# Kernel tuning notes

Measured on AMD Instinct MI355X. Metric: run time of the kernel, lower is better.

The kernel has to match this reference:

```python
import jax, jax.numpy as jnp
import numpy as np

N = 50000      # nodes
E = 800000     # edges
D_IN = 128
D_OUT = 128
R = 8          # relation types
EPS = 1e-12    # F.normalize eps


def setup_inputs() -> dict:
    key = jax.random.key(0)
    ks = jax.random.split(key, 10)
    s_in = 1.0 / np.sqrt(D_IN)
    s_out = 1.0 / np.sqrt(D_OUT)
    return {
        "x": jax.random.normal(ks[0], (N, D_IN), jnp.float32),
        "W1": jax.random.normal(ks[1], (R, D_IN, D_OUT), jnp.float32) * s_in,
        "loopW1": jax.random.normal(ks[2], (D_IN, D_OUT), jnp.float32) * s_in,
        "b1": jax.random.normal(ks[3], (D_OUT,), jnp.float32) * 0.01,
        "W2": jax.random.normal(ks[4], (R, D_OUT, D_OUT), jnp.float32) * s_out,
        "loopW2": jax.random.normal(ks[5], (D_OUT, D_OUT), jnp.float32) * s_out,
        "b2": jax.random.normal(ks[6], (D_OUT,), jnp.float32) * 0.01,
        "src": jax.random.randint(ks[7], (E,), 0, N),
        "dst": jax.random.randint(ks[8], (E,), 0, N),
        "etypes": jax.random.randint(ks[9], (E,), 0, R),
    }


def rel_layer(x, src, dst, etypes, W, loopW, b):
    # transform every node by every relation: [R, N, D_out]
    xw = jnp.einsum('ni,rio->rno', x, W)
    # gather per-edge messages: [E, D_out]
    msg = xw[etypes, src]
    # scatter-add to destination nodes
    agg = jax.ops.segment_sum(msg, dst, num_segments=x.shape[0])
    # self-loop + bias (DGL RelGraphConv defaults)
    return agg + x @ loopW + b


def reference(x, W1, loopW1, b1, W2, loopW2, b2, src, dst, etypes):
    h = jax.nn.relu(rel_layer(x, src, dst, etypes, W1, loopW1, b1))
    h = rel_layer(h, src, dst, etypes, W2, loopW2, b2)
    # F.normalize: row-wise L2, eps=1e-12
    nrm = jnp.maximum(jnp.linalg.norm(h, axis=1, keepdims=True), EPS)
    return h / nrm
```

## Files before the change

### kernel.cpp

```cpp
#include <hip/hip_runtime.h>
#include <hip/hip_bf16.h>

#define D 128
#define CH 4096

typedef unsigned int u32;
typedef unsigned short u16;
typedef __attribute__((ext_vector_type(8))) short s16x8;
typedef __attribute__((ext_vector_type(4))) float f32x4;
typedef __attribute__((ext_vector_type(2))) float f32x2;

__device__ __forceinline__ float bf2f(u16 u) {
    union { u32 u; float f; } v; v.u = ((u32)u) << 16; return v.f;
}
__device__ __forceinline__ u16 f2bf(float f) {
    union { float f; u32 u; } v; v.f = f;
    return (u16)((v.u + 0x7fffu + ((v.u >> 16) & 1u)) >> 16);
}
__device__ __forceinline__ u32 pack_bf2(float a, float b) {
    __hip_bfloat162 t = __float22bfloat162_rn(make_float2(a, b));
    union { __hip_bfloat162 t; u32 u; } v; v.t = t; return v.u;
}
__device__ __forceinline__ void unpack2(u32 u, float& lo, float& hi) {
    union { u32 u; float f; } a, b;
    a.u = u << 16; b.u = u & 0xffff0000u;
    lo = a.f; hi = b.f;
}

__global__ void detect_dtype(const u16* __restrict__ x, int* __restrict__ flag) {
    __shared__ int cnt;
    if (threadIdx.x == 0) cnt = 0;
    __syncthreads();
    u16 u = x[2 * threadIdx.x];
    int e = (u >> 7) & 0xFF;
    if (e >= 96 && e <= 150) atomicAdd(&cnt, 1);
    __syncthreads();
    if (threadIdx.x == 0) *flag = (cnt >= 128) ? 0 : 1;
}

__global__ __launch_bounds__(256)
void to_bf16_all(const void* __restrict__ s0, const void* __restrict__ s1,
                 const void* __restrict__ s2, const void* __restrict__ s3,
                 const void* __restrict__ s4, const void* __restrict__ s5,
                 const void* __restrict__ s6,
                 u16* __restrict__ d0, u16* __restrict__ d1, u16* __restrict__ d2,
                 u16* __restrict__ d3, u16* __restrict__ d4, u16* __restrict__ d5,
                 u16* __restrict__ d6,
                 long long n0, long long n1, long long n2, long long n3,
                 long long n4, long long n5, long long n6,
                 const int* __restrict__ flag)
{
    if (*flag == 0) return;
    long long i = (long long)blockIdx.x * 256 + threadIdx.x;
    const void* s; u16* d; long long off;
    if      (i < n0)                   { s = s0; d = d0; off = i; }
    else if (i < n0+n1)                { s = s1; d = d1; off = i-n0; }
    else if (i < n0+n1+n2)             { s = s2; d = d2; off = i-n0-n1; }
    else if (i < n0+n1+n2+n3)          { s = s3; d = d3; off = i-n0-n1-n2; }
    else if (i < n0+n1+n2+n3+n4)       { s = s4; d = d4; off = i-n0-n1-n2-n3; }
    else if (i < n0+n1+n2+n3+n4+n5)    { s = s5; d = d5; off = i-n0-n1-n2-n3-n4; }
    else if (i < n0+n1+n2+n3+n4+n5+n6) { s = s6; d = d6; off = i-n0-n1-n2-n3-n4-n5; }
    else return;
    d[off] = f2bf(((const float*)s)[off]);
}

__global__ __launch_bounds__(256)
void zero_ints(int* __restrict__ a, int n) {
    int i = blockIdx.x * 256 + threadIdx.x;
    if (i < n) a[i] = 0;
}

__global__ __launch_bounds__(256)
void csr_count(const int* __restrict__ dst, int* __restrict__ gcnt, int E, int nbuck) {
    __shared__ int scnt[256];
    int tid = threadIdx.x;
    scnt[tid] = 0;
    __syncthreads();
    int base = blockIdx.x * CH;
#pragma unroll
    for (int it = 0; it < CH / 256; ++it) {
        int e = base + it * 256 + tid;
        if (e < E) atomicAdd(&scnt[dst[e] >> 8], 1);
    }
    __syncthreads();
    if (tid < nbuck && scnt[tid] > 0) atomicAdd(&gcnt[tid], scnt[tid]);
}

__global__ __launch_bounds__(256)
void csr_scan(const int* __restrict__ gcnt, int* __restrict__ bstart, int* __restrict__ bcur,
              int nbuck, int N_, int E_, int* __restrict__ offs) {
    __shared__ int wpart[4];
    int tid = threadIdx.x, lane = tid & 63, wid = tid >> 6;
    int v = (tid < nbuck) ? gcnt[tid] : 0;
    int s = v;
#pragma unroll
    for (int off = 1; off < 64; off <<= 1) {
        int t = __shfl_up(s, off, 64);
        if (lane >= off) s += t;
    }
    if (lane == 63) wpart[wid] = s;
    __syncthreads();
    int add = 0;
    for (int w = 0; w < wid; ++w) add += wpart[w];
    int excl = add + s - v;
    if (tid <= nbuck) bstart[tid] = excl;
    if (tid < nbuck)  bcur[tid]  = excl;
    if (tid == 0) offs[N_] = E_;
}

__global__ __launch_bounds__(256)
void csr_part(const int* __restrict__ src, const int* __restrict__ dst,
              const int* __restrict__ et, int* __restrict__ bcur,
              u32* __restrict__ ebuf, int E, int N, int nbuck) {
    __shared__ int scnt[256], sbase[256];
    int tid = threadIdx.x;
    scnt[tid] = 0;
    __syncthreads();
    int base = blockIdx.x * CH;
#pragma unroll
    for (int it = 0; it < CH / 256; ++it) {
        int e = base + it * 256 + tid;
        if (e < E) atomicAdd(&scnt[dst[e] >> 8], 1);
    }
    __syncthreads();
    if (tid < nbuck) {
        int c = scnt[tid];
        sbase[tid] = c ? atomicAdd(&bcur[tid], c) : 0;
    }
    __syncthreads();
    scnt[tid] = 0;
    __syncthreads();
#pragma unroll
    for (int it = 0; it < CH / 256; ++it) {
        int e = base + it * 256 + tid;
        if (e >= E) continue;
        int d = dst[e];
        int b = d >> 8;
        int p = sbase[b] + atomicAdd(&scnt[b], 1);
        ebuf[p] = ((u32)(d & 255) << 24) | (u32)(et[e] * N + src[e]);
    }
}

__global__ __launch_bounds__(256)
void csr_emit(const u32* __restrict__ ebuf, const int* __restrict__ bstart,
              int* __restrict__ offs, int* __restrict__ rowidx, int N) {
    __shared__ int hist[256], excl[256], cur[256];
    __shared__ int wpart[4];
    int b = blockIdx.x, tid = threadIdx.x;
    int lo = bstart[b], hi = bstart[b + 1];
    hist[tid] = 0; cur[tid] = 0;
    __syncthreads();
    for (int i = lo + tid; i < hi; i += 256) atomicAdd(&hist[ebuf[i] >> 24], 1);
    __syncthreads();
    int lane = tid & 63, wid = tid >> 6;
    int v = hist[tid], s = v;
#pragma unroll
    for (int off = 1; off < 64; off <<= 1) {
        int t = __shfl_up(s, off, 64);
        if (lane >= off) s += t;
    }
    if (lane == 63) wpart[wid] = s;
    __syncthreads();
    int add = 0;
    for (int w = 0; w < wid; ++w) add += wpart[w];
    int e_ = add + s - v;
    excl[tid] = e_;
    int node = (b << 8) + tid;
    if (node < N) offs[node] = lo + e_;
    __syncthreads();
    for (int i = lo + tid; i < hi; i += 256) {
        u32 rec = ebuf[i];
        int dl = rec >> 24;
        int p = lo + excl[dl] + atomicAdd(&cur[dl], 1);
        rowidx[p] = (int)(rec & 0xFFFFFFu);
    }
}

__global__ __launch_bounds__(256)
void gemm_k128(const u16* __restrict__ Ac, const u16* __restrict__ Ao,
               const u16* __restrict__ Wc, const u16* __restrict__ Wo,
               const u16* __restrict__ lWc, const u16* __restrict__ lWo,
               const u16* __restrict__ bc, const u16* __restrict__ bo,
               const int* __restrict__ flag,
               int M, int R_, u16* __restrict__ xw, u16* __restrict__ sl)
{
    __shared__ u16 As[128 * 128];
    const bool f = (*flag != 0);
    const u16* A     = f ? Ac  : Ao;
    const u16* Wall  = f ? Wc  : Wo;
    const u16* loopW = f ? lWc : lWo;
    const u16* bias  = f ? bc  : bo;

    const int y = blockIdx.y;
    const u16* B = (y < R_) ? (Wall + (long long)y * D * D) : loopW;
    const int row0 = blockIdx.x * 128;
    const int tid  = threadIdx.x;
    const int lane = tid & 63;
    const int wv   = tid >> 6;
    const int quad = lane >> 4;
    const int l16  = lane & 15;

    {
        int r_base = (wv << 2) + (lane >> 4);
        int c      = lane & 15;
        auto* lds0 = (__attribute__((address_space(3))) char*)As;
#pragma unroll
        for (int it = 0; it < 8; ++it) {
            int rl = it * 16 + r_base;
            int cg = c ^ (rl & 15);
            int rg = row0 + rl; if (rg >= M) rg = M - 1;
            const u16* gp = A + (long long)rg * D + cg * 8;
            __builtin_amdgcn_global_load_lds(
                (const __attribute__((address_space(1))) void*)gp,
                (__attribute__((address_space(3))) void*)(lds0 + it * 4096 + wv * 1024),
                16, 0, 0);
        }
    }

    s16x8 bf[4][2];
#pragma unroll
    for (int kk = 0; kk < 4; ++kk)
#pragma unroll
        for (int j = 0; j < 8; ++j) {
            u32 p = *(const u32*)(B + (kk * 32 + quad * 8 + j) * D + wv * 32 + 2 * l16);
            bf[kk][0][j] = (short)(p & 0xffffu);
            bf[kk][1][j] = (short)(p >> 16);
        }

    f32x4 acc[8][2];
#pragma unroll
    for (int mt = 0; mt < 8; ++mt) { acc[mt][0] = (f32x4)0.f; acc[mt][1] = (f32x4)0.f; }

    __syncthreads();

#pragma unroll
    for (int kk = 0; kk < 4; ++kk) {
        const int chunk = (kk * 4 + quad) ^ l16;
#pragma unroll
        for (int mt = 0; mt < 8; ++mt) {
            int rl = mt * 16 + l16;
            s16x8 a = *(const s16x8*)(As + rl * D + chunk * 8);
            acc[mt][0] = __builtin_amdgcn_mfma_f32_16x16x32_bf16(a, bf[kk][0], acc[mt][0], 0, 0, 0);
            acc[mt][1] = __builtin_amdgcn_mfma_f32_16x16x32_bf16(a, bf[kk][1], acc[mt][1], 0, 0, 0);
        }
    }

    long long MD64 = (long long)M * 64;
    int cpair = wv * 16 + l16;
    if (y < R_) {
        u32* o = (u32*)xw + (long long)y * MD64;
#pragma unroll
        for (int mt = 0; mt < 8; ++mt)
#pragma unroll
            for (int i = 0; i < 4; ++i) {
                int r = row0 + mt * 16 + quad * 4 + i;
                if (r >= M) continue;
                o[(long long)r * 64 + cpair] = pack_bf2(acc[mt][0][i], acc[mt][1][i]);
            }
    } else {
        float b0 = bf2f(bias[wv * 32 + 2 * l16]);
        float b1 = bf2f(bias[wv * 32 + 2 * l16 + 1]);
        u32* o = (u32*)sl;
#pragma unroll
        for (int mt = 0; mt < 8; ++mt)
#pragma unroll
            for (int i = 0; i < 4; ++i) {
                int r = row0 + mt * 16 + quad * 4 + i;
                if (r >= M) continue;
                o[(long long)r * 64 + cpair] = pack_bf2(acc[mt][0][i] + b0, acc[mt][1][i] + b1);
            }
    }
}

__global__ __launch_bounds__(256)
void aggregate(const u16* __restrict__ xw, const u16* __restrict__ sl,
               const int* __restrict__ offs, const int* __restrict__ rowidx,
               void* __restrict__ out, int N, int mode, const int* __restrict__ flag)
{
    int node = blockIdx.x * 4 + (threadIdx.x >> 6);
    int p = threadIdx.x & 63;
    if (node >= N) return;
    const u32* xw32 = (const u32*)xw;

    float a0, a1;
    unpack2(((const u32*)sl)[(long long)node * 64 + p], a0, a1);

    int j = offs[node], end = offs[node + 1];
    for (; j + 4 <= end; j += 4) {
        int r0 = rowidx[j], r1 = rowidx[j + 1], r2 = rowidx[j + 2], r3 = rowidx[j + 3];
        u32 u0 = xw32[(long long)r0 * 64 + p];
        u32 u1 = xw32[(long long)r1 * 64 + p];
        u32 u2 = xw32[(long long)r2 * 64 + p];
        u32 u3 = xw32[(long long)r3 * 64 + p];
        float l, h;
        unpack2(u0, l, h); a0 += l; a1 += h;
        unpack2(u1, l, h); a0 += l; a1 += h;
        unpack2(u2, l, h); a0 += l; a1 += h;
        unpack2(u3, l, h); a0 += l; a1 += h;
    }
    for (; j < end; ++j) {
        float l, h;
        unpack2(xw32[(long long)rowidx[j] * 64 + p], l, h);
        a0 += l; a1 += h;
    }

    if (mode == 0) {
        a0 = fmaxf(a0, 0.f); a1 = fmaxf(a1, 0.f);
        ((u32*)out)[(long long)node * 64 + p] = pack_bf2(a0, a1);
    } else {
        float s = a0 * a0 + a1 * a1;
#pragma unroll
        for (int off = 32; off > 0; off >>= 1) s += __shfl_xor(s, off, 64);
        float sc = 1.f / fmaxf(sqrtf(s), 1e-12f);
        a0 *= sc; a1 *= sc;
        if (*flag) {
            f32x2 w; w[0] = a0; w[1] = a1;
            ((f32x2*)out)[(long long)node * 64 + p] = w;
        } else {
            ((u32*)out)[(long long)node * 64 + p] = pack_bf2(a0, a1);
        }
    }
}

static inline size_t align256(size_t x) { return (x + 255) & ~(size_t)255; }

extern "C" void kernel_launch(void* const* d_in, const int* in_sizes, int n_in,
                              void* d_out, int out_size, void* d_ws, size_t ws_size,
                              hipStream_t stream)
{
    const void* x_in   = d_in[0];
    const void* W1_in  = d_in[1];
    const void* lW1_in = d_in[2];
    const void* b1_in  = d_in[3];
    const void* W2_in  = d_in[4];
    const void* lW2_in = d_in[5];
    const void* b2_in  = d_in[6];
    const int* src = (const int*)d_in[7];
    const int* dst = (const int*)d_in[8];
    const int* et  = (const int*)d_in[9];

    const int N = in_sizes[0] / D;
    const int E = in_sizes[7];
    const int R = in_sizes[1] / (D * D);
    const int nbuck = (N + 255) >> 8;

    const long long ND  = (long long)N * D;
    const long long RDD = (long long)R * D * D;
    const long long DDl = (long long)D * D;

    size_t off = 0;
    auto alloc = [&](size_t bytes) { size_t o = off; off = align256(off + bytes); return o; };
    size_t o_flag = alloc(256);
    size_t o_xc   = alloc((size_t)ND * 2);
    size_t o_W1   = alloc((size_t)RDD * 2);
    size_t o_lW1  = alloc((size_t)DDl * 2);
    size_t o_b1   = alloc((size_t)D * 2);
    size_t o_W2   = alloc((size_t)RDD * 2);
    size_t o_lW2  = alloc((size_t)DDl * 2);
    size_t o_b2   = alloc((size_t)D * 2);
    size_t o_sl   = alloc((size_t)ND * 2);
    size_t o_h    = alloc((size_t)ND * 2);
    size_t o_offs = alloc((size_t)(N + 1) * 4);
    size_t o_gcnt = alloc(1024);
    size_t o_bst  = alloc(1040 * 4);
    size_t o_bcur = alloc(1024);
    size_t o_ebuf = alloc((size_t)E * 4);
    size_t o_ridx = alloc((size_t)E * 4);
    size_t o_xw   = alloc((size_t)R * ND * 2);
    (void)ws_size;

    char* ws = (char*)d_ws;
    int* flag   = (int*)(ws + o_flag);
    u16* x_c    = (u16*)(ws + o_xc);
    u16* W1c    = (u16*)(ws + o_W1);
    u16* lW1c   = (u16*)(ws + o_lW1);
    u16* b1c    = (u16*)(ws + o_b1);
    u16* W2c    = (u16*)(ws + o_W2);
    u16* lW2c   = (u16*)(ws + o_lW2);
    u16* b2c    = (u16*)(ws + o_b2);
    u16* sl     = (u16*)(ws + o_sl);
    u16* h      = (u16*)(ws + o_h);
    int* offs   = (int*)(ws + o_offs);
    int* gcnt   = (int*)(ws + o_gcnt);
    int* bstart = (int*)(ws + o_bst);
    int* bcur   = (int*)(ws + o_bcur);
    u32* ebuf   = (u32*)(ws + o_ebuf);
    int* rowidx = (int*)(ws + o_ridx);
    u16* xw     = (u16*)(ws + o_xw);

    dim3 blk(256, 1, 1);
    int mb   = (N + 127) / 128;
    int nblkE = (E + CH - 1) / CH;
    auto cdiv = [](long long n) { return (u32)((n + 255) / 256); };

    detect_dtype<<<dim3(1), blk, 0, stream>>>((const u16*)x_in, flag);
    long long tot = ND + RDD + DDl + D + RDD + DDl + D;
    to_bf16_all<<<dim3(cdiv(tot)), blk, 0, stream>>>(
        x_in, W1_in, lW1_in, b1_in, W2_in, lW2_in, b2_in,
        x_c, W1c, lW1c, b1c, W2c, lW2c, b2c,
        ND, RDD, DDl, (long long)D, RDD, DDl, (long long)D, flag);

    zero_ints<<<dim3(1), blk, 0, stream>>>(gcnt, nbuck);
    csr_count<<<dim3(nblkE), blk, 0, stream>>>(dst, gcnt, E, nbuck);
    csr_scan<<<dim3(1), blk, 0, stream>>>(gcnt, bstart, bcur, nbuck, N, E, offs);
    csr_part<<<dim3(nblkE), blk, 0, stream>>>(src, dst, et, bcur, ebuf, E, N, nbuck);
    csr_emit<<<dim3(nbuck), blk, 0, stream>>>(ebuf, bstart, offs, rowidx, N);

    gemm_k128<<<dim3(mb, R + 1), blk, 0, stream>>>(
        x_c, (const u16*)x_in, W1c, (const u16*)W1_in, lW1c, (const u16*)lW1_in,
        b1c, (const u16*)b1_in, flag, N, R, xw, sl);
    aggregate<<<dim3((N + 3) / 4), blk, 0, stream>>>(xw, sl, offs, rowidx, h, N, 0, flag);

    gemm_k128<<<dim3(mb, R + 1), blk, 0, stream>>>(
        h, h, W2c, (const u16*)W2_in, lW2c, (const u16*)lW2_in,
        b2c, (const u16*)b2_in, flag, N, R, xw, sl);
    aggregate<<<dim3((N + 3) / 4), blk, 0, stream>>>(xw, sl, offs, rowidx, d_out, N, 1, flag);
}
```

Measured before the change: 303.6 us.

## Aggregate inputs per relation before transform and fuse gather-GEMM-normalize

Builds a CSR keyed by (destination, relation) and, per 128-node tile, sums raw neighbor features for each relation into LDS, then multiplies by that relation's weight with MFMA, accumulating alongside the self-loop term. This removes the R×N×D transformed-feature buffer and the separate aggregate kernels, cutting memory traffic. Bias, relu and the final L2 normalization are applied in the same kernel epilogue. It trades this for a serialized per-thread gather with a large register array, fewer blocks, and higher LDS use, which reduce occupancy.

```diff
diff --git a/kernel.cpp b/kernel.cpp
--- a/kernel.cpp
+++ b/kernel.cpp
@@ -9,6 +9,7 @@
 typedef __attribute__((ext_vector_type(8))) short s16x8;
 typedef __attribute__((ext_vector_type(4))) float f32x4;
 typedef __attribute__((ext_vector_type(2))) float f32x2;
+typedef __attribute__((ext_vector_type(4))) u32 u32x4;
 
 __device__ __forceinline__ float bf2f(u16 u) {
     union { u32 u; float f; } v; v.u = ((u32)u) << 16; return v.f;
@@ -88,7 +89,7 @@
 
 __global__ __launch_bounds__(256)
 void csr_scan(const int* __restrict__ gcnt, int* __restrict__ bstart, int* __restrict__ bcur,
-              int nbuck, int N_, int E_, int* __restrict__ offs) {
+              int nbuck, int NR, int E_, int* __restrict__ offs2) {
     __shared__ int wpart[4];
     int tid = threadIdx.x, lane = tid & 63, wid = tid >> 6;
     int v = (tid < nbuck) ? gcnt[tid] : 0;
@@ -105,13 +106,13 @@
     int excl = add + s - v;
     if (tid <= nbuck) bstart[tid] = excl;
     if (tid < nbuck)  bcur[tid]  = excl;
-    if (tid == 0) offs[N_] = E_;
+    if (tid == 0) offs2[NR] = E_;
 }
 
 __global__ __launch_bounds__(256)
 void csr_part(const int* __restrict__ src, const int* __restrict__ dst,
               const int* __restrict__ et, int* __restrict__ bcur,
-              u32* __restrict__ ebuf, int E, int N, int nbuck) {
+              u32* __restrict__ ebuf, int E, int nbuck) {
     __shared__ int scnt[256], sbase[256];
     int tid = threadIdx.x;
     scnt[tid] = 0;
@@ -137,79 +138,90 @@
         int d = dst[e];
         int b = d >> 8;
         int p = sbase[b] + atomicAdd(&scnt[b], 1);
-        ebuf[p] = ((u32)(d & 255) << 24) | (u32)(et[e] * N + src[e]);
-    }
-}
-
-__global__ __launch_bounds__(256)
-void csr_emit(const u32* __restrict__ ebuf, const int* __restrict__ bstart,
-              int* __restrict__ offs, int* __restrict__ rowidx, int N) {
-    __shared__ int hist[256], excl[256], cur[256];
+        ebuf[p] = ((u32)(d & 255) << 24) | ((u32)et[e] << 21) | (u32)src[e];
+    }
+}
+
+__global__ __launch_bounds__(256)
+void csr_emit2(const u32* __restrict__ ebuf, const int* __restrict__ bstart,
+               int* __restrict__ offs2, int* __restrict__ rowidx2, int N, int R_) {
+    __shared__ int hist[2048];
+    __shared__ int cur[2048];
     __shared__ int wpart[4];
+    __shared__ int carry_s;
     int b = blockIdx.x, tid = threadIdx.x;
     int lo = bstart[b], hi = bstart[b + 1];
-    hist[tid] = 0; cur[tid] = 0;
-    __syncthreads();
-    for (int i = lo + tid; i < hi; i += 256) atomicAdd(&hist[ebuf[i] >> 24], 1);
+    for (int k = tid; k < 2048; k += 256) { hist[k] = 0; cur[k] = 0; }
+    if (tid == 0) carry_s = 0;
+    __syncthreads();
+    for (int i = lo + tid; i < hi; i += 256) atomicAdd(&hist[ebuf[i] >> 21], 1);
     __syncthreads();
     int lane = tid & 63, wid = tid >> 6;
-    int v = hist[tid], s = v;
-#pragma unroll
-    for (int off = 1; off < 64; off <<= 1) {
-        int t = __shfl_up(s, off, 64);
-        if (lane >= off) s += t;
-    }
-    if (lane == 63) wpart[wid] = s;
-    __syncthreads();
-    int add = 0;
-    for (int w = 0; w < wid; ++w) add += wpart[w];
-    int e_ = add + s - v;
-    excl[tid] = e_;
-    int node = (b << 8) + tid;
-    if (node < N) offs[node] = lo + e_;
+    for (int c = 0; c < 8; ++c) {
+        int v = hist[c * 256 + tid];
+        int s = v;
+#pragma unroll
+        for (int off = 1; off < 64; off <<= 1) {
+            int t = __shfl_up(s, off, 64);
+            if (lane >= off) s += t;
+        }
+        if (lane == 63) wpart[wid] = s;
+        __syncthreads();
+        int add = 0;
+        for (int w = 0; w < wid; ++w) add += wpart[w];
+        int cbase = carry_s;
+        __syncthreads();
+        hist[c * 256 + tid] = cbase + add + s - v;
+        if (tid == 255) carry_s = cbase + add + s;
+        __syncthreads();
+    }
+    for (int k = tid; k < 2048; k += 256) {
+        int dlo = k >> 3, r = k & 7;
+        int d = (b << 8) + dlo;
+        if (d < N && r < R_) offs2[d * R_ + r] = lo + hist[k];
+    }
     __syncthreads();
     for (int i = lo + tid; i < hi; i += 256) {
         u32 rec = ebuf[i];
-        int dl = rec >> 24;
-        int p = lo + excl[dl] + atomicAdd(&cur[dl], 1);
-        rowidx[p] = (int)(rec & 0xFFFFFFu);
-    }
-}
-
-__global__ __launch_bounds__(256)
-void gemm_k128(const u16* __restrict__ Ac, const u16* __restrict__ Ao,
-               const u16* __restrict__ Wc, const u16* __restrict__ Wo,
-               const u16* __restrict__ lWc, const u16* __restrict__ lWo,
-               const u16* __restrict__ bc, const u16* __restrict__ bo,
-               const int* __restrict__ flag,
-               int M, int R_, u16* __restrict__ xw, u16* __restrict__ sl)
+        int key = rec >> 21;
+        int p = lo + hist[key] + atomicAdd(&cur[key], 1);
+        rowidx2[p] = (int)(rec & 0x1FFFFFu);
+    }
+}
+
+__global__ __launch_bounds__(256)
+void fused_layer(const u16* __restrict__ Xc, const u16* __restrict__ Xo,
+                 const u16* __restrict__ Wc, const u16* __restrict__ Wo,
+                 const u16* __restrict__ lWc, const u16* __restrict__ lWo,
+                 const u16* __restrict__ bc, const u16* __restrict__ bo,
+                 const int* __restrict__ flag,
+                 const int* __restrict__ offs2, const int* __restrict__ rowidx2,
+                 void* __restrict__ out, int M, int R_, int mode)
 {
-    __shared__ u16 As[128 * 128];
+    __shared__ u16 S[128 * 128];
+    __shared__ u16 SL[128 * 128];
     const bool f = (*flag != 0);
-    const u16* A     = f ? Ac  : Ao;
+    const u16* X     = f ? Xc  : Xo;
     const u16* Wall  = f ? Wc  : Wo;
     const u16* loopW = f ? lWc : lWo;
     const u16* bias  = f ? bc  : bo;
 
-    const int y = blockIdx.y;
-    const u16* B = (y < R_) ? (Wall + (long long)y * D * D) : loopW;
     const int row0 = blockIdx.x * 128;
     const int tid  = threadIdx.x;
-    const int lane = tid & 63;
-    const int wv   = tid >> 6;
-    const int quad = lane >> 4;
-    const int l16  = lane & 15;
+    const int lane = tid & 63, wv = tid >> 6, quad = lane >> 4, l16 = lane & 15;
+    const int d_loc = tid >> 1, half = tid & 1;
+    const int dg = row0 + d_loc;
 
     {
         int r_base = (wv << 2) + (lane >> 4);
         int c      = lane & 15;
-        auto* lds0 = (__attribute__((address_space(3))) char*)As;
+        auto* lds0 = (__attribute__((address_space(3))) char*)SL;
 #pragma unroll
         for (int it = 0; it < 8; ++it) {
             int rl = it * 16 + r_base;
             int cg = c ^ (rl & 15);
             int rg = row0 + rl; if (rg >= M) rg = M - 1;
-            const u16* gp = A + (long long)rg * D + cg * 8;
+            const u16* gp = X + (long long)rg * D + cg * 8;
             __builtin_amdgcn_global_load_lds(
                 (const __attribute__((address_space(1))) void*)gp,
                 (__attribute__((address_space(3))) void*)(lds0 + it * 4096 + wv * 1024),
@@ -217,107 +229,118 @@
         }
     }
 
-    s16x8 bf[4][2];
-#pragma unroll
-    for (int kk = 0; kk < 4; ++kk)
-#pragma unroll
-        for (int j = 0; j < 8; ++j) {
-            u32 p = *(const u32*)(B + (kk * 32 + quad * 8 + j) * D + wv * 32 + 2 * l16);
-            bf[kk][0][j] = (short)(p & 0xffffu);
-            bf[kk][1][j] = (short)(p >> 16);
+    f32x4 acc[8][2];
+#pragma unroll
+    for (int mt = 0; mt < 8; ++mt) { acc[mt][0] = (f32x4)0.f; acc[mt][1] = (f32x4)0.f; }
+
+    const u32* X32 = (const u32*)X;
+
+    for (int r = 0; r <= R_; ++r) {
+        const u16* B = (r < R_) ? (Wall + (long long)r * D * D) : loopW;
+        if (r < R_) {
+            float ga[64];
+#pragma unroll
+            for (int k = 0; k < 64; ++k) ga[k] = 0.f;
+            if (dg < M) {
+                int j0 = offs2[dg * R_ + r], j1 = offs2[dg * R_ + r + 1];
+                for (int j = j0; j < j1; ++j) {
+                    int s = rowidx2[j];
+                    const u32x4* xr = (const u32x4*)(X32 + (long long)s * 64 + half * 32);
+#pragma unroll
+                    for (int q = 0; q < 8; ++q) {
+                        u32x4 u = xr[q];
+#pragma unroll
+                        for (int m2 = 0; m2 < 4; ++m2) {
+                            float lo_, hi_;
+                            unpack2(u[m2], lo_, hi_);
+                            ga[(q * 4 + m2) * 2]     += lo_;
+                            ga[(q * 4 + m2) * 2 + 1] += hi_;
+                        }
+                    }
+                }
+            }
+            __syncthreads();
+#pragma unroll
+            for (int q = 0; q < 8; ++q) {
+                int g  = half * 8 + q;
+                int gs = g ^ (d_loc & 15);
+                u32x4 w;
+#pragma unroll
+                for (int m2 = 0; m2 < 4; ++m2)
+                    w[m2] = pack_bf2(ga[(q * 4 + m2) * 2], ga[(q * 4 + m2) * 2 + 1]);
+                *(u32x4*)((char*)S + d_loc * 256 + gs * 16) = w;
+            }
+            __syncthreads();
+        } else {
+            __syncthreads();
         }
-
-    f32x4 acc[8][2];
-#pragma unroll
-    for (int mt = 0; mt < 8; ++mt) { acc[mt][0] = (f32x4)0.f; acc[mt][1] = (f32x4)0.f; }
-
-    __syncthreads();
-
-#pragma unroll
-    for (int kk = 0; kk < 4; ++kk) {
-        const int chunk = (kk * 4 + quad) ^ l16;
-#pragma unroll
-        for (int mt = 0; mt < 8; ++mt) {
-            int rl = mt * 16 + l16;
-            s16x8 a = *(const s16x8*)(As + rl * D + chunk * 8);
-            acc[mt][0] = __builtin_amdgcn_mfma_f32_16x16x32_bf16(a, bf[kk][0], acc[mt][0], 0, 0, 0);
-            acc[mt][1] = __builtin_amdgcn_mfma_f32_16x16x32_bf16(a, bf[kk][1], acc[mt][1], 0, 0, 0);
+        const u16* As_ = (r < R_) ? S : SL;
+
+        s16x8 bf[4][2];
+#pragma unroll
+        for (int kk = 0; kk < 4; ++kk)
+#pragma unroll
+            for (int j = 0; j < 8; ++j) {
+                u32 p = *(const u32*)(B + (kk * 32 + quad * 8 + j) * D + wv * 32 + 2 * l16);
+                bf[kk][0][j] = (short)(p & 0xffffu);
+                bf[kk][1][j] = (short)(p >> 16);
+            }
+#pragma unroll
+        for (int kk = 0; kk < 4; ++kk) {
+            const int chunk = (kk * 4 + quad) ^ l16;
+#pragma unroll
+            for (int mt = 0; mt < 8; ++mt) {
+                int rl = mt * 16 + l16;
+                s16x8 a = *(const s16x8*)(As_ + rl * D + chunk * 8);
+                acc[mt][0] = __builtin_amdgcn_mfma_f32_16x16x32_bf16(a, bf[kk][0], acc[mt][0], 0, 0, 0);
+                acc[mt][1] = __builtin_amdgcn_mfma_f32_16x16x32_bf16(a, bf[kk][1], acc[mt][1], 0, 0, 0);
+            }
         }
     }
 
-    long long MD64 = (long long)M * 64;
+    float b0 = bf2f(bias[wv * 32 + 2 * l16]);
+    float b1 = bf2f(bias[wv * 32 + 2 * l16 + 1]);
     int cpair = wv * 16 + l16;
-    if (y < R_) {
-        u32* o = (u32*)xw + (long long)y * MD64;
+    if (mode == 0) {
+        u32* o = (u32*)out;
 #pragma unroll
         for (int mt = 0; mt < 8; ++mt)
 #pragma unroll
             for (int i = 0; i < 4; ++i) {
-                int r = row0 + mt * 16 + quad * 4 + i;
-                if (r >= M) continue;
-                o[(long long)r * 64 + cpair] = pack_bf2(acc[mt][0][i], acc[mt][1][i]);
+                int rr = row0 + mt * 16 + quad * 4 + i;
+                if (rr >= M) continue;
+                float v0 = fmaxf(acc[mt][0][i] + b0, 0.f);
+                float v1 = fmaxf(acc[mt][1][i] + b1, 0.f);
+                o[(long long)rr * 64 + cpair] = pack_bf2(v0, v1);
             }
     } else {
-        float b0 = bf2f(bias[wv * 32 + 2 * l16]);
-        float b1 = bf2f(bias[wv * 32 + 2 * l16 + 1]);
-        u32* o = (u32*)sl;
+        __syncthreads();
+        u32* T = (u32*)S;
 #pragma unroll
         for (int mt = 0; mt < 8; ++mt)
 #pragma unroll
             for (int i = 0; i < 4; ++i) {
-                int r = row0 + mt * 16 + quad * 4 + i;
-                if (r >= M) continue;
-                o[(long long)r * 64 + cpair] = pack_bf2(acc[mt][0][i] + b0, acc[mt][1][i] + b1);
-            }
-    }
-}
-
-__global__ __launch_bounds__(256)
-void aggregate(const u16* __restrict__ xw, const u16* __restrict__ sl,
-               const int* __restrict__ offs, const int* __restrict__ rowidx,
-               void* __restrict__ out, int N, int mode, const int* __restrict__ flag)
-{
-    int node = blockIdx.x * 4 + (threadIdx.x >> 6);
-    int p = threadIdx.x & 63;
-    if (node >= N) return;
-    const u32* xw32 = (const u32*)xw;
-
-    float a0, a1;
-    unpack2(((const u32*)sl)[(long long)node * 64 + p], a0, a1);
-
-    int j = offs[node], end = offs[node + 1];
-    for (; j + 4 <= end; j += 4) {
-        int r0 = rowidx[j], r1 = rowidx[j + 1], r2 = rowidx[j + 2], r3 = rowidx[j + 3];
-        u32 u0 = xw32[(long long)r0 * 64 + p];
-        u32 u1 = xw32[(long long)r1 * 64 + p];
-        u32 u2 = xw32[(long long)r2 * 64 + p];
-        u32 u3 = xw32[(long long)r3 * 64 + p];
-        float l, h;
-        unpack2(u0, l, h); a0 += l; a1 += h;
-        unpack2(u1, l, h); a0 += l; a1 += h;
-        unpack2(u2, l, h); a0 += l; a1 += h;
-        unpack2(u3, l, h); a0 += l; a1 += h;
-    }
-    for (; j < end; ++j) {
-        float l, h;
-        unpack2(xw32[(long long)rowidx[j] * 64 + p], l, h);
-        a0 += l; a1 += h;
-    }
-
-    if (mode == 0) {
-        a0 = fmaxf(a0, 0.f); a1 = fmaxf(a1, 0.f);
-        ((u32*)out)[(long long)node * 64 + p] = pack_bf2(a0, a1);
-    } else {
-        float s = a0 * a0 + a1 * a1;
-#pragma unroll
-        for (int off = 32; off > 0; off >>= 1) s += __shfl_xor(s, off, 64);
-        float sc = 1.f / fmaxf(sqrtf(s), 1e-12f);
-        a0 *= sc; a1 *= sc;
-        if (*flag) {
-            f32x2 w; w[0] = a0; w[1] = a1;
-            ((f32x2*)out)[(long long)node * 64 + p] = w;
-        } else {
-            ((u32*)out)[(long long)node * 64 + p] = pack_bf2(a0, a1);
+                int rl = mt * 16 + quad * 4 + i;
+                T[rl * 64 + cpair] = pack_bf2(acc[mt][0][i] + b0, acc[mt][1][i] + b1);
+            }
+        __syncthreads();
+        for (int rr = 0; rr < 32; ++rr) {
+            int rl = wv * 32 + rr;
+            int dgr = row0 + rl;
+            u32 u = T[rl * 64 + lane];
+            float a0, a1; unpack2(u, a0, a1);
+            float s = a0 * a0 + a1 * a1;
+#pragma unroll
+            for (int off = 32; off > 0; off >>= 1) s += __shfl_xor(s, off, 64);
+            float sc = 1.f / fmaxf(sqrtf(s), 1e-12f);
+            if (dgr < M) {
+                if (f) {
+                    f32x2 w; w[0] = a0 * sc; w[1] = a1 * sc;
+                    ((f32x2*)out)[(long long)dgr * 64 + lane] = w;
+                } else {
+                    ((u32*)out)[(long long)dgr * 64 + lane] = pack_bf2(a0 * sc, a1 * sc);
+                }
+            }
         }
     }
 }
@@ -342,11 +365,11 @@
     const int N = in_sizes[0] / D;
     const int E = in_sizes[7];
     const int R = in_sizes[1] / (D * D);
-    const int nbuck = (N + 255) >> 8;
 
     const long long ND  = (long long)N * D;
     const long long RDD = (long long)R * D * D;
     const long long DDl = (long long)D * D;
+    const int nbuck = (N + 255) >> 8;
 
     size_t off = 0;
     auto alloc = [&](size_t bytes) { size_t o = off; off = align256(off + bytes); return o; };
@@ -358,38 +381,34 @@
     size_t o_W2   = alloc((size_t)RDD * 2);
     size_t o_lW2  = alloc((size_t)DDl * 2);
     size_t o_b2   = alloc((size_t)D * 2);
-    size_t o_sl   = alloc((size_t)ND * 2);
     size_t o_h    = alloc((size_t)ND * 2);
-    size_t o_offs = alloc((size_t)(N + 1) * 4);
+    size_t o_off2 = alloc(((size_t)N * R + 1) * 4);
     size_t o_gcnt = alloc(1024);
     size_t o_bst  = alloc(1040 * 4);
     size_t o_bcur = alloc(1024);
     size_t o_ebuf = alloc((size_t)E * 4);
     size_t o_ridx = alloc((size_t)E * 4);
-    size_t o_xw   = alloc((size_t)R * ND * 2);
     (void)ws_size;
 
     char* ws = (char*)d_ws;
-    int* flag   = (int*)(ws + o_flag);
-    u16* x_c    = (u16*)(ws + o_xc);
-    u16* W1c    = (u16*)(ws + o_W1);
-    u16* lW1c   = (u16*)(ws + o_lW1);
-    u16* b1c    = (u16*)(ws + o_b1);
-    u16* W2c    = (u16*)(ws + o_W2);
-    u16* lW2c   = (u16*)(ws + o_lW2);
-    u16* b2c    = (u16*)(ws + o_b2);
-    u16* sl     = (u16*)(ws + o_sl);
-    u16* h      = (u16*)(ws + o_h);
-    int* offs   = (int*)(ws + o_offs);
-    int* gcnt   = (int*)(ws + o_gcnt);
-    int* bstart = (int*)(ws + o_bst);
-    int* bcur   = (int*)(ws + o_bcur);
-    u32* ebuf   = (u32*)(ws + o_ebuf);
-    int* rowidx = (int*)(ws + o_ridx);
-    u16* xw     = (u16*)(ws + o_xw);
+    int* flag    = (int*)(ws + o_flag);
+    u16* x_c     = (u16*)(ws + o_xc);
+    u16* W1c     = (u16*)(ws + o_W1);
+    u16* lW1c    = (u16*)(ws + o_lW1);
+    u16* b1c     = (u16*)(ws + o_b1);
+    u16* W2c     = (u16*)(ws + o_W2);
+    u16* lW2c    = (u16*)(ws + o_lW2);
+    u16* b2c     = (u16*)(ws + o_b2);
+    u16* h       = (u16*)(ws + o_h);
+    int* offs2   = (int*)(ws + o_off2);
+    int* gcnt    = (int*)(ws + o_gcnt);
+    int* bstart  = (int*)(ws + o_bst);
+    int* bcur    = (int*)(ws + o_bcur);
+    u32* ebuf    = (u32*)(ws + o_ebuf);
+    int* rowidx2 = (int*)(ws + o_ridx);
 
     dim3 blk(256, 1, 1);
-    int mb   = (N + 127) / 128;
+    int mb    = (N + 127) / 128;
     int nblkE = (E + CH - 1) / CH;
     auto cdiv = [](long long n) { return (u32)((n + 255) / 256); };
 
@@ -402,17 +421,15 @@
 
     zero_ints<<<dim3(1), blk, 0, stream>>>(gcnt, nbuck);
     csr_count<<<dim3(nblkE), blk, 0, stream>>>(dst, gcnt, E, nbuck);
-    csr_scan<<<dim3(1), blk, 0, stream>>>(gcnt, bstart, bcur, nbuck, N, E, offs);
-    csr_part<<<dim3(nblkE), blk, 0, stream>>>(src, dst, et, bcur, ebuf, E, N, nbuck);
-    csr_emit<<<dim3(nbuck), blk, 0, stream>>>(ebuf, bstart, offs, rowidx, N);
-
-    gemm_k128<<<dim3(mb, R + 1), blk, 0, stream>>>(
+    csr_scan<<<dim3(1), blk, 0, stream>>>(gcnt, bstart, bcur, nbuck, N * R, E, offs2);
+    csr_part<<<dim3(nblkE), blk, 0, stream>>>(src, dst, et, bcur, ebuf, E, nbuck);
+    csr_emit2<<<dim3(nbuck), blk, 0, stream>>>(ebuf, bstart, offs2, rowidx2, N, R);
+
+    fused_layer<<<dim3(mb), blk, 0, stream>>>(
         x_c, (const u16*)x_in, W1c, (const u16*)W1_in, lW1c, (const u16*)lW1_in,
-        b1c, (const u16*)b1_in, flag, N, R, xw, sl);
-    aggregate<<<dim3((N + 3) / 4), blk, 0, stream>>>(xw, sl, offs, rowidx, h, N, 0, flag);
-
-    gemm_k128<<<dim3(mb, R + 1), blk, 0, stream>>>(
+        b1c, (const u16*)b1_in, flag, offs2, rowidx2, h, N, R, 0);
+
+    fused_layer<<<dim3(mb), blk, 0, stream>>>(
         h, h, W2c, (const u16*)W2_in, lW2c, (const u16*)lW2_in,
-        b2c, (const u16*)b2_in, flag, N, R, xw, sl);
-    aggregate<<<dim3((N + 3) / 4), blk, 0, stream>>>(xw, sl, offs, rowidx, d_out, N, 1, flag);
-}
+        b2c, (const u16*)b2_in, flag, offs2, rowidx2, d_out, N, R, 1);
+}
```

After: 340.3 us. 12.1% more time.
